# Performance work log

Measured on AMD Instinct MI355X. Metric: run time of the kernel, lower is better.

Reference implementation:

```python
import jax, jax.numpy as jnp
import numpy as np

L = 3          # num_gc_layers
DIM = 128      # hidden dim (== num_features)
BN_EPS = 1e-5


def _bn(h, gamma, beta):
    # torch BatchNorm1d training-mode normalization (biased variance)
    m = h.mean(axis=0)
    v = h.var(axis=0)
    return gamma * (h - m) * jax.lax.rsqrt(v + BN_EPS) + beta


def setup_inputs() -> dict:
    key = jax.random.key(0)
    ks = jax.random.split(key, 24)
    N, E, G = 50000, 600000, 256
    s = 0.05
    inp = {
        "x": jax.random.normal(ks[0], (N, DIM), jnp.float32),
        "src": jax.random.randint(ks[1], (E,), 0, N, jnp.int32),
        "dst": jax.random.randint(ks[2], (E,), 0, N, jnp.int32),
        "batch": jnp.sort(jax.random.randint(ks[3], (N,), 0, G, jnp.int32)),
        "n_graphs": G,
        # GIN MLP params (stacked over layers; num_features == dim)
        "conv_w1": jax.random.normal(ks[4], (L, DIM, DIM), jnp.float32) * s,
        "conv_b1": jnp.zeros((L, DIM), jnp.float32),
        "conv_w2": jax.random.normal(ks[5], (L, DIM, DIM), jnp.float32) * s,
        "conv_b2": jnp.zeros((L, DIM), jnp.float32),
        "bn_gamma": jnp.ones((L, DIM), jnp.float32),
        "bn_beta": jnp.zeros((L, DIM), jnp.float32),
        # summary weighter (dim -> 1)
        "sw_w": jax.random.normal(ks[6], (DIM, 1), jnp.float32) * s,
        "sw_b": jnp.zeros((1,), jnp.float32),
        # VAE heads
        "nmu_w": jax.random.normal(ks[7], (DIM, DIM), jnp.float32) * s,
        "nmu_b": jnp.zeros((DIM,), jnp.float32),
        "nlv_w": jax.random.normal(ks[8], (DIM, DIM), jnp.float32) * s,
        "nlv_b": jnp.zeros((DIM,), jnp.float32),
        "gmu_w": jax.random.normal(ks[9], (DIM, DIM), jnp.float32) * s,
        "gmu_b": jnp.zeros((DIM,), jnp.float32),
        "glv_w": jax.random.normal(ks[10], (DIM, DIM), jnp.float32) * s,
        "glv_b": jnp.zeros((DIM,), jnp.float32),
        # head BN params, order: [node_mu, node_logvar, graph_mu, graph_logvar]
        "head_gamma": jnp.ones((4, DIM), jnp.float32),
        "head_beta": jnp.zeros((4, DIM), jnp.float32),
    }
    return inp


def reference(x, src, dst, batch, n_graphs,
              conv_w1, conv_b1, conv_w2, conv_b2, bn_gamma, bn_beta,
              sw_w, sw_b, nmu_w, nmu_b, nlv_w, nlv_b,
              gmu_w, gmu_b, glv_w, glv_b, head_gamma, head_beta):
    N = x.shape[0]
    for i in range(L):
        # GINConv (eps=0): h = nn(x + sum_{j->i} x_j)
        agg = jax.ops.segment_sum(x[src], dst, num_segments=N)  # [N, dim]
        h = x + agg
        h = jax.nn.relu(h @ conv_w1[i] + conv_b1[i]) @ conv_w2[i] + conv_b2[i]
        x = _bn(jax.nn.relu(h), bn_gamma[i], bn_beta[i])

    w = jax.nn.sigmoid(x @ sw_w + sw_b)           # [N, 1]
    summary_info = w * x                          # [N, dim]
    noisy_info = (1.0 - w) * x                    # [N, dim]
    slots = jax.ops.segment_sum(summary_info, batch, num_segments=n_graphs)  # [G, dim]

    node_mu = _bn(jax.nn.relu(noisy_info @ nmu_w + nmu_b), head_gamma[0], head_beta[0])
    node_logvar = _bn(jax.nn.relu(noisy_info @ nlv_w + nlv_b), head_gamma[1], head_beta[1])
    graph_mu = _bn(jax.nn.relu(slots @ gmu_w + gmu_b), head_gamma[2], head_beta[2])
    graph_logvar = _bn(jax.nn.relu(slots @ glv_w + glv_b), head_gamma[3], head_beta[3])
    return (node_mu, node_logvar, graph_mu, graph_logvar)
```

## Files before the change

### kernel.cpp

```cpp
#include <hip/hip_runtime.h>
#include <hip/hip_bf16.h>

#define DIM 128
#define BN_EPS 1e-5f
#define NSTRIPE 32

typedef unsigned short ushortT;
typedef __attribute__((ext_vector_type(8))) short short8;
typedef __attribute__((ext_vector_type(4))) float floatx4;

__device__ __forceinline__ float bflo(unsigned u) { return __uint_as_float(u << 16); }
__device__ __forceinline__ float bfhi(unsigned u) { return __uint_as_float(u & 0xffff0000u); }
__device__ __forceinline__ float bf2f(ushortT h) { return __uint_as_float(((unsigned)h) << 16); }
__device__ __forceinline__ ushortT f2bf(float f) {
    unsigned x = __float_as_uint(f);
    unsigned r = (x + 0x7fff + ((x >> 16) & 1)) >> 16;
    return (ushortT)r;
}
__device__ __forceinline__ void decode8(const unsigned* ap, short8& hi, short8& lo) {
#pragma unroll
    for (int j = 0; j < 8; ++j) {
        hi[j] = (short)(ap[j] >> 16);
        lo[j] = (short)(ap[j] & 0xffffu);
    }
// ... 183 lines not shown
                const ushortT* sp = Xb + (size_t)eidx[i] * DIM + c0;
                acc8(&acc[0], *(const uint4*)(sp));
                acc8(&acc[8], *(const uint4*)(sp + 8));
            }
            if (sprev) {
                float cnt = (float)(e - b + 1);
#pragma unroll
                for (int jq = 0; jq < 4; ++jq) {
                    int c = c0 + jq * 4;
                    float4 sm = *(const float4*)&pstat[c];
                    float4 sq = *(const float4*)&pstat[128 + c];
                    float4 gm = *(const float4*)(gamma + c);
                    float4 bt = *(const float4*)(beta + c);
                    float m, sc;
                    m = sm.x * invM; sc = gm.x * rsqrtf(sq.x * invM - m * m + BN_EPS);
                    acc[jq * 4 + 0] = sc * acc[jq * 4 + 0] + cnt * (bt.x - sc * m);
                    m = sm.y * invM; sc = gm.y * rsqrtf(sq.y * invM - m * m + BN_EPS);
                    acc[jq * 4 + 1] = sc * acc[jq * 4 + 1] + cnt * (bt.y - sc * m);
                    m = sm.z * invM; sc = gm.z * rsqrtf(sq.z * invM - m * m + BN_EPS);
                    acc[jq * 4 + 2] = sc * acc[jq * 4 + 2] + cnt * (bt.z - sc * m);
                    m = sm.w * invM; sc = gm.w * rsqrtf(sq.w * invM - m * m + BN_EPS);
                    acc[jq * 4 + 3] = sc * acc[jq * 4 + 3] + cnt * (bt.w - sc * m);
                }
            }
        }
        unsigned pk[16];
#pragma unroll
        for (int j = 0; j < 16; ++j) {
            ushortT h = f2bf(acc[j]);
            ushortT l = f2bf(acc[j] - bf2f(h));
            pk[j] = ((unsigned)h << 16) | l;
        }
#pragma unroll
        for (int j4 = 0; j4 < 4; ++j4)
            *(uint4*)&As[nloc][c0 + j4 * 4] = *(uint4*)&pk[j4 * 4];
    }
    __syncthreads();

    int cbase = wave * 32;
    floatx4 acc[2][2];
#pragma unroll
    for (int mt = 0; mt < 2; ++mt)
#pragma unroll
        for (int nt = 0; nt < 2; ++nt)
            acc[mt][nt] = (floatx4){0.f, 0.f, 0.f, 0.f};

#pragma unroll
    for (int ks = 0; ks < 4; ++ks) {
        int k0 = ks * 32 + quad * 8;
        short8 bhi[2], blo[2];
#pragma unroll
        for (int nt = 0; nt < 2; ++nt) {
            const size_t woff = (size_t)(cbase + nt * 16 + l16) * DIM + k0;
            bhi[nt] = *(const short8*)(W1hi + woff);
            blo[nt] = *(const short8*)(W1lo + woff);
        }
#pragma unroll
        for (int mt = 0; mt < 2; ++mt) {
            int lr = mt * 16 + l16;
            unsigned ap[8];
            *(uint4*)&ap[0] = *(const uint4*)&As[lr][k0];
            *(uint4*)&ap[4] = *(const uint4*)&As[lr][k0 + 4];
            short8 ahi, alo;
            decode8(ap, ahi, alo);
#pragma unroll
            for (int nt = 0; nt < 2; ++nt) {
                acc[mt][nt] = __builtin_amdgcn_mfma_f32_16x16x32_bf16(ahi, bhi[nt], acc[mt][nt], 0, 0, 0);
                acc[mt][nt] = __builtin_amdgcn_mfma_f32_16x16x32_bf16(alo, bhi[nt], acc[mt][nt], 0, 0, 0);
                acc[mt][nt] = __builtin_amdgcn_mfma_f32_16x16x32_bf16(ahi, blo[nt], acc[mt][nt], 0, 0, 0);
            }
        }
    }
    __syncthreads();

#pragma unroll
    for (int nt = 0; nt < 2; ++nt) {
        int col = cbase + nt * 16 + l16;
        float bcol = b1[col];
#pragma unroll
        for (int mt = 0; mt < 2; ++mt)
#pragma unroll
            for (int r = 0; r < 4; ++r) {
                int lr = mt * 16 + quad * 4 + r;
                float v = fmaxf(acc[mt][nt][r] + bcol, 0.f);
                ushortT hv = f2bf(v);
                ushortT lv = f2bf(v - bf2f(hv));
                As[lr][col] = ((unsigned)hv << 16) | lv;
            }
    }
    __syncthreads();

#pragma unroll
    for (int mt = 0; mt < 2; ++mt)
#pragma unroll
        for (int nt = 0; nt < 2; ++nt)
            acc[mt][nt] = (floatx4){0.f, 0.f, 0.f, 0.f};

#pragma unroll
    for (int ks = 0; ks < 4; ++ks) {
        int k0 = ks * 32 + quad * 8;
        short8 bhi[2], blo[2];
#pragma unroll
        for (int nt = 0; nt < 2; ++nt) {
            const size_t woff = (size_t)(cbase + nt * 16 + l16) * DIM + k0;
            bhi[nt] = *(const short8*)(W2hi + woff);
            blo[nt] = *(const short8*)(W2lo + woff);
        }
#pragma unroll
        for (int mt = 0; mt < 2; ++mt) {
            int lr = mt * 16 + l16;
            unsigned ap[8];
            *(uint4*)&ap[0] = *(const uint4*)&As[lr][k0];
            *(uint4*)&ap[4] = *(const uint4*)&As[lr][k0 + 4];
            short8 ahi, alo;
            decode8(ap, ahi, alo);
#pragma unroll
            for (int nt = 0; nt < 2; ++nt) {
                acc[mt][nt] = __builtin_amdgcn_mfma_f32_16x16x32_bf16(ahi, bhi[nt], acc[mt][nt], 0, 0, 0);
                acc[mt][nt] = __builtin_amdgcn_mfma_f32_16x16x32_bf16(alo, bhi[nt], acc[mt][nt], 0, 0, 0);
                acc[mt][nt] = __builtin_amdgcn_mfma_f32_16x16x32_bf16(ahi, blo[nt], acc[mt][nt], 0, 0, 0);
            }
        }
    }
#pragma unroll
    for (int nt = 0; nt < 2; ++nt) {
        int col = cbase + nt * 16 + l16;
        float bcol = b2[col];
        float s = 0.f, sq = 0.f;
#pragma unroll
        for (int mt = 0; mt < 2; ++mt)
#pragma unroll
            for (int r = 0; r < 4; ++r) {
                int gr = m0 + mt * 16 + quad * 4 + r;
                if (gr < M) {
                    float v = fmaxf(acc[mt][nt][r] + bcol, 0.f);
                    rout[(size_t)gr * DIM + col] = f2bf(v);
                    s += v;
                    sq += v * v;
                }
            }
        s  += __shfl_xor(s, 16);  s  += __shfl_xor(s, 32);
        sq += __shfl_xor(sq, 16); sq += __shfl_xor(sq, 32);
        if (quad == 0) {
            atomicAdd(&ls[col], s);
            atomicAdd(&lsq[col], sq);
        }
    }
    __syncthreads();
    float* dstp = sdst + (size_t)(blockIdx.x & (NSTRIPE - 1)) * 256;
    if (t < 128) atomicAdd(&dstp[t], ls[t]);
    else         atomicAdd(&dstp[t], lsq[t - 128]);
}

__global__ __launch_bounds__(256) void heads_kernel(
    const unsigned* __restrict__ AP,
    const ushortT* __restrict__ WAhi, const ushortT* __restrict__ WAlo,
    const float* __restrict__ bA, ushortT* __restrict__ hA, float* __restrict__ sdstA,
    const ushortT* __restrict__ WBhi, const ushortT* __restrict__ WBlo,
    const float* __restrict__ bB, ushortT* __restrict__ hB, float* __restrict__ sdstB,
    int M)
{
    __shared__ float lsA[DIM], lsqA[DIM], lsB[DIM], lsqB[DIM];
    int t = threadIdx.x;
    int wave = t >> 6, lane = t & 63, quad = lane >> 4, l16 = lane & 15;
    int m0 = blockIdx.x * 64;
    int cbase = wave * 32;

    if (t < DIM) { lsA[t] = 0.f; lsqA[t] = 0.f; lsB[t] = 0.f; lsqB[t] = 0.f; }
    __syncthreads();

    floatx4 accA[4][2], accB[4][2];
#pragma unroll
    for (int mt = 0; mt < 4; ++mt)
#pragma unroll
        for (int nt = 0; nt < 2; ++nt) {
            accA[mt][nt] = (floatx4){0.f, 0.f, 0.f, 0.f};
            accB[mt][nt] = (floatx4){0.f, 0.f, 0.f, 0.f};
        }

    for (int ks = 0; ks < 4; ++ks) {
        int k0 = ks * 32 + quad * 8;
        short8 bAhi[2], bAlo[2], bBhi[2], bBlo[2];
#pragma unroll
        for (int nt = 0; nt < 2; ++nt) {
            const size_t woff = (size_t)(cbase + nt * 16 + l16) * DIM + k0;
            bAhi[nt] = *(const short8*)(WAhi + woff);
            bAlo[nt] = *(const short8*)(WAlo + woff);
            bBhi[nt] = *(const short8*)(WBhi + woff);
            bBlo[nt] = *(const short8*)(WBlo + woff);
        }
#pragma unroll
        for (int mt = 0; mt < 4; ++mt) {
            int row = m0 + mt * 16 + l16;
            unsigned ap[8] = {0, 0, 0, 0, 0, 0, 0, 0};
            if (row < M) {
                *(uint4*)&ap[0] = *(const uint4*)(AP + (size_t)row * DIM + k0);
                *(uint4*)&ap[4] = *(const uint4*)(AP + (size_t)row * DIM + k0 + 4);
            }
            short8 ahi, alo;
            decode8(ap, ahi, alo);
#pragma unroll
            for (int nt = 0; nt < 2; ++nt) {
                accA[mt][nt] = __builtin_amdgcn_mfma_f32_16x16x32_bf16(ahi, bAhi[nt], accA[mt][nt], 0, 0, 0);
                accA[mt][nt] = __builtin_amdgcn_mfma_f32_16x16x32_bf16(alo, bAhi[nt], accA[mt][nt], 0, 0, 0);
                accA[mt][nt] = __builtin_amdgcn_mfma_f32_16x16x32_bf16(ahi, bAlo[nt], accA[mt][nt], 0, 0, 0);
                accB[mt][nt] = __builtin_amdgcn_mfma_f32_16x16x32_bf16(ahi, bBhi[nt], accB[mt][nt], 0, 0, 0);
                accB[mt][nt] = __builtin_amdgcn_mfma_f32_16x16x32_bf16(alo, bBhi[nt], accB[mt][nt], 0, 0, 0);
                accB[mt][nt] = __builtin_amdgcn_mfma_f32_16x16x32_bf16(ahi, bBlo[nt], accB[mt][nt], 0, 0, 0);
            }
        }
    }

#pragma unroll
    for (int nt = 0; nt < 2; ++nt) {
        int col = cbase + nt * 16 + l16;
        float bcA = bA[col], bcB = bB[col];
        float sA = 0.f, sqA = 0.f, sB = 0.f, sqB = 0.f;
#pragma unroll
        for (int mt = 0; mt < 4; ++mt)
#pragma unroll
            for (int r = 0; r < 4; ++r) {
                int gr = m0 + mt * 16 + quad * 4 + r;
                if (gr < M) {
                    size_t off = (size_t)gr * DIM + col;
                    float vA = fmaxf(accA[mt][nt][r] + bcA, 0.f);
                    float vB = fmaxf(accB[mt][nt][r] + bcB, 0.f);
                    hA[off] = f2bf(vA);
                    hB[off] = f2bf(vB);
                    sA += vA; sqA += vA * vA;
                    sB += vB; sqB += vB * vB;
                }
            }
        sA += __shfl_xor(sA, 16);  sA += __shfl_xor(sA, 32);
        sqA += __shfl_xor(sqA, 16); sqA += __shfl_xor(sqA, 32);
        sB += __shfl_xor(sB, 16);  sB += __shfl_xor(sB, 32);
        sqB += __shfl_xor(sqB, 16); sqB += __shfl_xor(sqB, 32);
        if (quad == 0) {
            atomicAdd(&lsA[col], sA);
            atomicAdd(&lsqA[col], sqA);
            atomicAdd(&lsB[col], sB);
            atomicAdd(&lsqB[col], sqB);
        }
    }
    __syncthreads();
    int stripe = blockIdx.x & (NSTRIPE - 1);
    float* dA = sdstA + (size_t)stripe * 256;
    float* dB = sdstB + (size_t)stripe * 256;
    if (t < 128) { atomicAdd(&dA[t], lsA[t]); atomicAdd(&dB[t], lsB[t]); }
    else         { atomicAdd(&dA[t], lsqA[t - 128]); atomicAdd(&dB[t], lsqB[t - 128]); }
}

__global__ __launch_bounds__(256) void merge_stats2_kernel(
    const float* __restrict__ sA, float* __restrict__ oA,
    const float* __restrict__ sB, float* __restrict__ oB)
{
    const float* s = blockIdx.x ? sB : sA;
    float* o = blockIdx.x ? oB : oA;
    int t = threadIdx.x;
    float v = 0.f;
#pragma unroll
    for (int i = 0; i < NSTRIPE; ++i) v += s[i * 256 + t];
    o[t] = v;
}

__global__ __launch_bounds__(256) void gemm_graph_dual_kernel(
    const float* __restrict__ A32,
    const ushortT* __restrict__ W8hi, const ushortT* __restrict__ W8lo,
    const float* __restrict__ b8, float* __restrict__ C8, float* __restrict__ st8,
    const ushortT* __restrict__ W9hi, const ushortT* __restrict__ W9lo,
    const float* __restrict__ b9, float* __restrict__ C9, float* __restrict__ st9,
    int M, int nb)
{
    __shared__ float ls[DIM], lsq[DIM];
    int bb = blockIdx.x;
    const ushortT* Whi; const ushortT* Wlo; const float* bias; float* C; float* st;
    if (bb < nb) { Whi = W8hi; Wlo = W8lo; bias = b8; C = C8; st = st8; }
    else { bb -= nb; Whi = W9hi; Wlo = W9lo; bias = b9; C = C9; st = st9; }

    int t     = threadIdx.x;
    int wave  = t >> 6;
    int lane  = t & 63;
    int quad  = lane >> 4;
    int l16   = lane & 15;
    int m0    = bb * 64;
    int cbase = wave * 32;

    if (t < DIM) { ls[t] = 0.f; lsq[t] = 0.f; }
    __syncthreads();

    floatx4 acc[4][2];
#pragma unroll
    for (int mt = 0; mt < 4; ++mt)
#pragma unroll
        for (int nt = 0; nt < 2; ++nt)
            acc[mt][nt] = (floatx4){0.f, 0.f, 0.f, 0.f};

    for (int ks = 0; ks < 4; ++ks) {
        int k0 = ks * 32 + quad * 8;
        short8 bhi[2], blo[2];
#pragma unroll
        for (int nt = 0; nt < 2; ++nt) {
            const size_t woff = (size_t)(cbase + nt * 16 + l16) * DIM + k0;
            bhi[nt] = *(const short8*)(Whi + woff);
            blo[nt] = *(const short8*)(Wlo + woff);
        }
#pragma unroll
        for (int mt = 0; mt < 4; ++mt) {
            int row = m0 + mt * 16 + l16;
            short8 ahi = {0,0,0,0,0,0,0,0};
            short8 alo = {0,0,0,0,0,0,0,0};
            if (row < M) {
                float av[8];
                *(float4*)&av[0] = *(const float4*)(A32 + (size_t)row * DIM + k0);
                *(float4*)&av[4] = *(const float4*)(A32 + (size_t)row * DIM + k0 + 4);
#pragma unroll
                for (int j = 0; j < 8; ++j) {
                    ushortT hv = f2bf(av[j]);
                    ahi[j] = (short)hv;
                    alo[j] = (short)f2bf(av[j] - bf2f(hv));
                }
            }
#pragma unroll
            for (int nt = 0; nt < 2; ++nt) {
                acc[mt][nt] = __builtin_amdgcn_mfma_f32_16x16x32_bf16(ahi, bhi[nt], acc[mt][nt], 0, 0, 0);
                acc[mt][nt] = __builtin_amdgcn_mfma_f32_16x16x32_bf16(alo, bhi[nt], acc[mt][nt], 0, 0, 0);
                acc[mt][nt] = __builtin_amdgcn_mfma_f32_16x16x32_bf16(ahi, blo[nt], acc[mt][nt], 0, 0, 0);
            }
        }
    }

#pragma unroll
    for (int nt = 0; nt < 2; ++nt) {
        int col = cbase + nt * 16 + l16;
        float bcol = bias[col];
        float s = 0.f, sq = 0.f;
#pragma unroll
        for (int mt = 0; mt < 4; ++mt)
#pragma unroll
            for (int r = 0; r < 4; ++r) {
                int gr = m0 + mt * 16 + quad * 4 + r;
                if (gr < M) {
                    float v = fmaxf(acc[mt][nt][r] + bcol, 0.f);
                    C[(size_t)gr * DIM + col] = v;
                    s += v;
                    sq += v * v;
                }
            }
        s  += __shfl_xor(s, 16);  s  += __shfl_xor(s, 32);
        sq += __shfl_xor(sq, 16); sq += __shfl_xor(sq, 32);
        if (quad == 0) {
            atomicAdd(&ls[col], s);
            atomicAdd(&lsq[col], sq);
        }
    }
    __syncthreads();
    if (t < DIM) {
        atomicAdd(&st[t], ls[t]);
        atomicAdd(&st[DIM + t], lsq[t]);
    }
}

__global__ __launch_bounds__(256) void bn_dual_bf16_kernel(
    const ushortT* __restrict__ RA, float* __restrict__ OA, const float* __restrict__ stA,
    const float* __restrict__ gA, const float* __restrict__ bA,
    const ushortT* __restrict__ RB, float* __restrict__ OB, const float* __restrict__ stB,
    const float* __restrict__ gB, const float* __restrict__ bB,
    int M, int nb)
{
    int bb = blockIdx.x;
    const ushortT* R; float* O; const float* st; const float* gamma; const float* beta;
    if (bb < nb) { R = RA; O = OA; st = stA; gamma = gA; beta = bA; }
    else { bb -= nb; R = RB; O = OB; st = stB; gamma = gB; beta = bB; }
    int idx = bb * 256 + threadIdx.x;
    if (idx >= M * 32) return;
    int c4 = idx & 31;
    float invM = 1.0f / (float)M;
    uint2 u = ((const uint2*)R)[idx];
    float o[4] = {bflo(u.x), bfhi(u.x), bflo(u.y), bfhi(u.y)};
#pragma unroll
    for (int j = 0; j < 4; ++j) {
        int c = c4 * 4 + j;
        float m   = st[c] * invM;
        float var = st[DIM + c] * invM - m * m;
        float sc  = gamma[c] * rsqrtf(var + BN_EPS);
        o[j] = sc * (o[j] - m) + beta[c];
    }
    ((float4*)O)[idx] = make_float4(o[0], o[1], o[2], o[3]);
}

__global__ __launch_bounds__(256) void bn_dual_f32_kernel(
    float* __restrict__ CA, const float* __restrict__ stA,
    const float* __restrict__ gA, const float* __restrict__ bA,
    float* __restrict__ CB, const float* __restrict__ stB,
    const float* __restrict__ gB, const float* __restrict__ bB,
    int M, int nb)
{
    int bb = blockIdx.x;
    float* C; const float* st; const float* gamma; const float* beta;
    if (bb < nb) { C = CA; st = stA; gamma = gA; beta = bA; }
    else { bb -= nb; C = CB; st = stB; gamma = gB; beta = bB; }
    int idx = bb * 256 + threadIdx.x;
    if (idx >= M * 32) return;
    int c4 = idx & 31;
    float invM = 1.0f / (float)M;
    float4 v = ((const float4*)C)[idx];
    float o[4] = {v.x, v.y, v.z, v.w};
#pragma unroll
    for (int j = 0; j < 4; ++j) {
        int c = c4 * 4 + j;
        float m   = st[c] * invM;
        float var = st[DIM + c] * invM - m * m;
        float sc  = gamma[c] * rsqrtf(var + BN_EPS);
        o[j] = sc * (o[j] - m) + beta[c];
    }
    ((float4*)C)[idx] = make_float4(o[0], o[1], o[2], o[3]);
}

__global__ __launch_bounds__(256) void weigh_split_kernel(
    const ushortT* __restrict__ R, const int* __restrict__ batch,
    const float* __restrict__ sprev,
    const float* __restrict__ gamma, const float* __restrict__ beta,
    const float* __restrict__ sw_w, const float* __restrict__ sw_b,
    unsigned* __restrict__ noisyP, float* __restrict__ slots, int N, float invM)
{
    __shared__ float part[256];
    __shared__ float wsh[128];
    __shared__ float pstat[256];
    int t  = threadIdx.x;
    int r0 = blockIdx.x * 128;

    {
        float s = 0.f;
#pragma unroll
        for (int i = 0; i < NSTRIPE; ++i) s += sprev[i * 256 + t];
        pstat[t] = s;
    }
    __syncthreads();

    {
        int row  = r0 + (t >> 1);
        int cs   = (t & 1) * 64;
        float d = 0.f;
        if (row < N) {
            for (int c = cs; c < cs + 64; c += 4) {
                uint2 u = *(const uint2*)(R + (size_t)row * DIM + c);
                float rv[4] = {bflo(u.x), bfhi(u.x), bflo(u.y), bfhi(u.y)};
                float4 sm = *(const float4*)&pstat[c];
                float4 sq = *(const float4*)&pstat[128 + c];
                float4 gm = *(const float4*)(gamma + c);
                float4 bt = *(const float4*)(beta + c);
                float4 sw = *(const float4*)(sw_w + c);
                float m, sc;
                m = sm.x * invM; sc = gm.x * rsqrtf(sq.x * invM - m * m + BN_EPS);
                d += (sc * (rv[0] - m) + bt.x) * sw.x;
                m = sm.y * invM; sc = gm.y * rsqrtf(sq.y * invM - m * m + BN_EPS);
                d += (sc * (rv[1] - m) + bt.y) * sw.y;
                m = sm.z * invM; sc = gm.z * rsqrtf(sq.z * invM - m * m + BN_EPS);
                d += (sc * (rv[2] - m) + bt.z) * sw.z;
                m = sm.w * invM; sc = gm.w * rsqrtf(sq.w * invM - m * m + BN_EPS);
                d += (sc * (rv[3] - m) + bt.w) * sw.w;
            }
        }
        part[t] = d;
    }
    __syncthreads();
    if (t < 128) {
        float dd = part[2 * t] + part[2 * t + 1];
        wsh[t] = 1.0f / (1.0f + expf(-(dd + sw_b[0])));
    }
    __syncthreads();

    int c    = t & 127;
    int half = t >> 7;
    int rend = r0 + 128;
    if (rend > N) rend = N;
    float m   = pstat[c] * invM;
    float var = pstat[128 + c] * invM - m * m;
    float sc  = gamma[c] * rsqrtf(var + BN_EPS);
    float sh  = beta[c] - sc * m;
    int curg = -1;
    float acc = 0.f;
    for (int r = r0 + half; r < rend; r += 2) {
        float xv = sc * bf2f(R[(size_t)r * DIM + c]) + sh;
        float w  = wsh[r - r0];
        float nv = (1.f - w) * xv;
        ushortT hv = f2bf(nv);
        ushortT lv = f2bf(nv - bf2f(hv));
        noisyP[(size_t)r * DIM + c] = ((unsigned)hv << 16) | lv;
        int g = batch[r];
        if (g != curg) {
            if (curg >= 0) atomicAdd(&slots[(size_t)curg * DIM + c], acc);
            curg = g;
            acc = 0.f;
        }
        acc += w * xv;
    }
    if (curg >= 0) atomicAdd(&slots[(size_t)curg * DIM + c], acc);
}

extern "C" void kernel_launch(void* const* d_in, const int* in_sizes, int n_in,
                              void* d_out, int out_size, void* d_ws, size_t ws_size,
                              hipStream_t stream)
{
    const float* x      = (const float*)d_in[0];
    const int*   src    = (const int*)d_in[1];
    const int*   dst    = (const int*)d_in[2];
    const int*   batch  = (const int*)d_in[3];
    const float* cw1    = (const float*)d_in[5];
    const float* cb1    = (const float*)d_in[6];
    const float* cw2    = (const float*)d_in[7];
    const float* cb2    = (const float*)d_in[8];
    const float* bng    = (const float*)d_in[9];
    const float* bnb    = (const float*)d_in[10];
    const float* sw_w   = (const float*)d_in[11];
    const float* sw_b   = (const float*)d_in[12];
    const float* nmu_b  = (const float*)d_in[14];
    const float* nlv_b  = (const float*)d_in[16];
    const float* gmu_b  = (const float*)d_in[18];
    const float* glv_b  = (const float*)d_in[20];
    const float* hgam   = (const float*)d_in[21];
    const float* hbet   = (const float*)d_in[22];
    const float* nmu_w  = (const float*)d_in[13];
    const float* nlv_w  = (const float*)d_in[15];
    const float* gmu_w  = (const float*)d_in[17];
    const float* glv_w  = (const float*)d_in[19];

    const int N = in_sizes[0] / DIM;
    const int E = in_sizes[1];
    const int G = (out_size / DIM - 2 * N) / 2;

    float* out0 = (float*)d_out;
    float* out1 = out0 + (size_t)N * DIM;
    float* out2 = out1 + (size_t)N * DIM;
    float* out3 = out2 + (size_t)G * DIM;

    char* wp = (char*)d_ws;
    auto alloc = [&](size_t bytes) {
        char* p = wp;
        wp += (bytes + 255) & ~(size_t)255;
        return p;
    };
    ushortT*  xbf   = (ushortT*)alloc((size_t)N * DIM * 2);
    ushortT*  rA    = (ushortT*)alloc((size_t)N * DIM * 2);
    ushortT*  rB    = (ushortT*)alloc((size_t)N * DIM * 2);
    unsigned* noisyP= (unsigned*)alloc((size_t)N * DIM * 4);
    ushortT*  whi   = (ushortT*)alloc((size_t)10 * 16384 * 2);
    ushortT*  wlo   = (ushortT*)alloc((size_t)10 * 16384 * 2);
    float* slots    = (float*)alloc((size_t)G * DIM * 4);
    float* stats    = (float*)alloc((size_t)7 * 256 * 4);
    float* sbuf     = (float*)alloc((size_t)5 * NSTRIPE * 256 * 4);
    int* row_ptr    = (int*)alloc((size_t)(N + 2) * 4);
    int* eidx       = (int*)alloc((size_t)E * 4);
    int* deg   = (int*)noisyP;
    int* iscan = deg + N;
    int* bsum  = iscan + N;
    int* cur   = bsum + 256;

    auto SS = [&](int i) { return stats + (size_t)i * 256; };
    auto SB = [&](int i) { return sbuf + (size_t)i * NSTRIPE * 256; };

    const int edge_blocks  = (E + 255) / 256;
    const int scan_blocks  = (N + 255) / 256;
    const int layer_blocks = (N + 31) / 32;
    const int heads_blocks = (N + 63) / 64;
    const int g16_blocks   = (N * 16 + 255) / 256;
    const int g32_blocks   = (N * 32 + 255) / 256;
    const float invN = 1.0f / (float)N;

    const int sbufQ  = (5 * NSTRIPE * 256) / 4;
    const int slotsQ = (G * DIM) / 4;
    const int degQ   = (N + 3) / 4;
    const int statsQ = (7 * 256) / 4;
    const int zeroQ  = sbufQ + slotsQ + degQ + statsQ;
    const int zero_blocks = (zeroQ + 255) / 256;

    prep_kernel<<<640 + g16_blocks + zero_blocks, 256, 0, stream>>>(
        cw1, cw2, nmu_w, nlv_w, gmu_w, glv_w, whi, wlo,
        x, xbf, N * 16, g16_blocks,
        (float4*)sbuf, sbufQ, (float4*)slots, slotsQ,
        (float4*)deg, degQ, (float4*)stats, statsQ);

    hist_kernel<<<edge_blocks, 256, 0, stream>>>(dst, deg, E);
    scan1_kernel<<<scan_blocks, 256, 0, stream>>>(deg, iscan, bsum, N);
    scan2_kernel<<<1, 256, 0, stream>>>(bsum, scan_blocks);
    scan3_kernel<<<scan_blocks, 256, 0, stream>>>(iscan, bsum, deg, row_ptr, cur, N);
    fill_kernel<<<edge_blocks, 256, 0, stream>>>(src, dst, cur, eidx, E);

    const ushortT* lin[3]  = {xbf, rA, rB};
    ushortT*       lout[3] = {rA, rB, rA};
    for (int l = 0; l < 3; ++l) {
        const float* sprev  = (l == 0) ? nullptr : SB(l - 1);
        const float* g_prev = (l == 0) ? nullptr : bng + (size_t)(l - 1) * DIM;
        const float* b_prev = (l == 0) ? nullptr : bnb + (size_t)(l - 1) * DIM;
        layer_fused_kernel<<<layer_blocks, 256, 0, stream>>>(
            lin[l], row_ptr, eidx,
            sprev, g_prev, b_prev,
            whi + (size_t)l * 16384, wlo + (size_t)l * 16384, cb1 + (size_t)l * DIM,
            whi + (size_t)(3 + l) * 16384, wlo + (size_t)(3 + l) * 16384, cb2 + (size_t)l * DIM,
            lout[l], SB(l), N, invN);
    }
    ushortT* rfin = rA;
    ushortT* hA   = rB;
    ushortT* hB   = xbf;

    weigh_split_kernel<<<(N + 127) / 128, 256, 0, stream>>>(
        rfin, batch, SB(2), bng + 2 * DIM, bnb + 2 * DIM,
        sw_w, sw_b, noisyP, slots, N, invN);

    heads_kernel<<<heads_blocks, 256, 0, stream>>>(
        noisyP,
        whi + (size_t)6 * 16384, wlo + (size_t)6 * 16384, nmu_b, hA, SB(3),
        whi + (size_t)7 * 16384, wlo + (size_t)7 * 16384, nlv_b, hB, SB(4), N);
    merge_stats2_kernel<<<2, 256, 0, stream>>>(SB(3), SS(3), SB(4), SS(4));
    bn_dual_bf16_kernel<<<2 * g32_blocks, 256, 0, stream>>>(
        hA, out0, SS(3), hgam + 0 * DIM, hbet + 0 * DIM,
        hB, out1, SS(4), hgam + 1 * DIM, hbet + 1 * DIM, N, g32_blocks);

    const int gemm_blocks_G = (G + 63) / 64;
    const int gbn_blocks    = (G * 32 + 255) / 256;
    gemm_graph_dual_kernel<<<2 * gemm_blocks_G, 256, 0, stream>>>(
        slots,
        whi + (size_t)8 * 16384, wlo + (size_t)8 * 16384, gmu_b, out2, SS(5),
        whi + (size_t)9 * 16384, wlo + (size_t)9 * 16384, glv_b, out3, SS(6),
        G, gemm_blocks_G);
    bn_dual_f32_kernel<<<2 * gbn_blocks, 256, 0, stream>>>(
        out2, SS(5), hgam + 2 * DIM, hbet + 2 * DIM,
        out3, SS(6), hgam + 3 * DIM, hbet + 3 * DIM, G, gbn_blocks);
}
```

Baseline: 470.1 us.

## Fuse summary weighting into node head GEMM via shared-memory noisy tile

Merges the weigh/split kernel into the node-head GEMM kernel: each 64-row block computes the BN-normalized final features, the sigmoid weights and the slot sums, then writes the hi/lo-packed noisy features into an LDS tile that feeds the MFMA GEMM directly. This removes the global noisyP round trip (a 50000x128 uint32 write plus read) and one kernel launch. In exchange it uses a larger LDS footprint (about 34KB per block), which may reduce occupancy. It also halves the rows per block in the weighting phase, which doubles the per-block stripe-stat reduction and slot atomics.

```diff
diff --git a/kernel.cpp b/kernel.cpp
--- a/kernel.cpp
+++ b/kernel.cpp
@@ -359,282 +359,26 @@
     else         atomicAdd(&dstp[t], lsq[t - 128]);
 }
 
-__global__ __launch_bounds__(256) void heads_kernel(
-    const unsigned* __restrict__ AP,
+__global__ __launch_bounds__(256) void weigh_heads_kernel(
+    const ushortT* __restrict__ R, const int* __restrict__ batch,
+    const float* __restrict__ sprev,
+    const float* __restrict__ gamma, const float* __restrict__ beta,
+    const float* __restrict__ sw_w, const float* __restrict__ sw_b,
+    float* __restrict__ slots,
     const ushortT* __restrict__ WAhi, const ushortT* __restrict__ WAlo,
     const float* __restrict__ bA, ushortT* __restrict__ hA, float* __restrict__ sdstA,
     const ushortT* __restrict__ WBhi, const ushortT* __restrict__ WBlo,
     const float* __restrict__ bB, ushortT* __restrict__ hB, float* __restrict__ sdstB,
-    int M)
-{
+    int N, float invM)
+{
+    __shared__ unsigned As[64][DIM + 4];
+    __shared__ float pstat[256];
+    __shared__ float part[256];
+    __shared__ float wsh[64];
     __shared__ float lsA[DIM], lsqA[DIM], lsB[DIM], lsqB[DIM];
     int t = threadIdx.x;
     int wave = t >> 6, lane = t & 63, quad = lane >> 4, l16 = lane & 15;
     int m0 = blockIdx.x * 64;
-    int cbase = wave * 32;
-
-    if (t < DIM) { lsA[t] = 0.f; lsqA[t] = 0.f; lsB[t] = 0.f; lsqB[t] = 0.f; }
-    __syncthreads();
-
-    floatx4 accA[4][2], accB[4][2];
-#pragma unroll
-    for (int mt = 0; mt < 4; ++mt)
-#pragma unroll
-        for (int nt = 0; nt < 2; ++nt) {
-            accA[mt][nt] = (floatx4){0.f, 0.f, 0.f, 0.f};
-            accB[mt][nt] = (floatx4){0.f, 0.f, 0.f, 0.f};
-        }
-
-    for (int ks = 0; ks < 4; ++ks) {
-        int k0 = ks * 32 + quad * 8;
-        short8 bAhi[2], bAlo[2], bBhi[2], bBlo[2];
-#pragma unroll
-        for (int nt = 0; nt < 2; ++nt) {
-            const size_t woff = (size_t)(cbase + nt * 16 + l16) * DIM + k0;
-            bAhi[nt] = *(const short8*)(WAhi + woff);
-            bAlo[nt] = *(const short8*)(WAlo + woff);
-            bBhi[nt] = *(const short8*)(WBhi + woff);
-            bBlo[nt] = *(const short8*)(WBlo + woff);
-        }
-#pragma unroll
-        for (int mt = 0; mt < 4; ++mt) {
-            int row = m0 + mt * 16 + l16;
-            unsigned ap[8] = {0, 0, 0, 0, 0, 0, 0, 0};
-            if (row < M) {
-                *(uint4*)&ap[0] = *(const uint4*)(AP + (size_t)row * DIM + k0);
-                *(uint4*)&ap[4] = *(const uint4*)(AP + (size_t)row * DIM + k0 + 4);
-            }
-            short8 ahi, alo;
-            decode8(ap, ahi, alo);
-#pragma unroll
-            for (int nt = 0; nt < 2; ++nt) {
-                accA[mt][nt] = __builtin_amdgcn_mfma_f32_16x16x32_bf16(ahi, bAhi[nt], accA[mt][nt], 0, 0, 0);
-                accA[mt][nt] = __builtin_amdgcn_mfma_f32_16x16x32_bf16(alo, bAhi[nt], accA[mt][nt], 0, 0, 0);
-                accA[mt][nt] = __builtin_amdgcn_mfma_f32_16x16x32_bf16(ahi, bAlo[nt], accA[mt][nt], 0, 0, 0);
-                accB[mt][nt] = __builtin_amdgcn_mfma_f32_16x16x32_bf16(ahi, bBhi[nt], accB[mt][nt], 0, 0, 0);
-                accB[mt][nt] = __builtin_amdgcn_mfma_f32_16x16x32_bf16(alo, bBhi[nt], accB[mt][nt], 0, 0, 0);
-                accB[mt][nt] = __builtin_amdgcn_mfma_f32_16x16x32_bf16(ahi, bBlo[nt], accB[mt][nt], 0, 0, 0);
-            }
-        }
-    }
-
-#pragma unroll
-    for (int nt = 0; nt < 2; ++nt) {
-        int col = cbase + nt * 16 + l16;
-        float bcA = bA[col], bcB = bB[col];
-        float sA = 0.f, sqA = 0.f, sB = 0.f, sqB = 0.f;
-#pragma unroll
-        for (int mt = 0; mt < 4; ++mt)
-#pragma unroll
-            for (int r = 0; r < 4; ++r) {
-                int gr = m0 + mt * 16 + quad * 4 + r;
-                if (gr < M) {
-                    size_t off = (size_t)gr * DIM + col;
-                    float vA = fmaxf(accA[mt][nt][r] + bcA, 0.f);
-                    float vB = fmaxf(accB[mt][nt][r] + bcB, 0.f);
-                    hA[off] = f2bf(vA);
-                    hB[off] = f2bf(vB);
-                    sA += vA; sqA += vA * vA;
-                    sB += vB; sqB += vB * vB;
-                }
-            }
-        sA += __shfl_xor(sA, 16);  sA += __shfl_xor(sA, 32);
-        sqA += __shfl_xor(sqA, 16); sqA += __shfl_xor(sqA, 32);
-        sB += __shfl_xor(sB, 16);  sB += __shfl_xor(sB, 32);
-        sqB += __shfl_xor(sqB, 16); sqB += __shfl_xor(sqB, 32);
-        if (quad == 0) {
-            atomicAdd(&lsA[col], sA);
-            atomicAdd(&lsqA[col], sqA);
-            atomicAdd(&lsB[col], sB);
-            atomicAdd(&lsqB[col], sqB);
-        }
-    }
-    __syncthreads();
-    int stripe = blockIdx.x & (NSTRIPE - 1);
-    float* dA = sdstA + (size_t)stripe * 256;
-    float* dB = sdstB + (size_t)stripe * 256;
-    if (t < 128) { atomicAdd(&dA[t], lsA[t]); atomicAdd(&dB[t], lsB[t]); }
-    else         { atomicAdd(&dA[t], lsqA[t - 128]); atomicAdd(&dB[t], lsqB[t - 128]); }
-}
-
-__global__ __launch_bounds__(256) void merge_stats2_kernel(
-    const float* __restrict__ sA, float* __restrict__ oA,
-    const float* __restrict__ sB, float* __restrict__ oB)
-{
-    const float* s = blockIdx.x ? sB : sA;
-    float* o = blockIdx.x ? oB : oA;
-    int t = threadIdx.x;
-    float v = 0.f;
-#pragma unroll
-    for (int i = 0; i < NSTRIPE; ++i) v += s[i * 256 + t];
-    o[t] = v;
-}
-
-__global__ __launch_bounds__(256) void gemm_graph_dual_kernel(
-    const float* __restrict__ A32,
-    const ushortT* __restrict__ W8hi, const ushortT* __restrict__ W8lo,
-    const float* __restrict__ b8, float* __restrict__ C8, float* __restrict__ st8,
-    const ushortT* __restrict__ W9hi, const ushortT* __restrict__ W9lo,
-    const float* __restrict__ b9, float* __restrict__ C9, float* __restrict__ st9,
-    int M, int nb)
-{
-    __shared__ float ls[DIM], lsq[DIM];
-    int bb = blockIdx.x;
-    const ushortT* Whi; const ushortT* Wlo; const float* bias; float* C; float* st;
-    if (bb < nb) { Whi = W8hi; Wlo = W8lo; bias = b8; C = C8; st = st8; }
-    else { bb -= nb; Whi = W9hi; Wlo = W9lo; bias = b9; C = C9; st = st9; }
-
-    int t     = threadIdx.x;
-    int wave  = t >> 6;
-    int lane  = t & 63;
-    int quad  = lane >> 4;
-    int l16   = lane & 15;
-    int m0    = bb * 64;
-    int cbase = wave * 32;
-
-    if (t < DIM) { ls[t] = 0.f; lsq[t] = 0.f; }
-    __syncthreads();
-
-    floatx4 acc[4][2];
-#pragma unroll
-    for (int mt = 0; mt < 4; ++mt)
-#pragma unroll
-        for (int nt = 0; nt < 2; ++nt)
-            acc[mt][nt] = (floatx4){0.f, 0.f, 0.f, 0.f};
-
-    for (int ks = 0; ks < 4; ++ks) {
-        int k0 = ks * 32 + quad * 8;
-        short8 bhi[2], blo[2];
-#pragma unroll
-        for (int nt = 0; nt < 2; ++nt) {
-            const size_t woff = (size_t)(cbase + nt * 16 + l16) * DIM + k0;
-            bhi[nt] = *(const short8*)(Whi + woff);
-            blo[nt] = *(const short8*)(Wlo + woff);
-        }
-#pragma unroll
-        for (int mt = 0; mt < 4; ++mt) {
-            int row = m0 + mt * 16 + l16;
-            short8 ahi = {0,0,0,0,0,0,0,0};
-            short8 alo = {0,0,0,0,0,0,0,0};
-            if (row < M) {
-                float av[8];
-                *(float4*)&av[0] = *(const float4*)(A32 + (size_t)row * DIM + k0);
-                *(float4*)&av[4] = *(const float4*)(A32 + (size_t)row * DIM + k0 + 4);
-#pragma unroll
-                for (int j = 0; j < 8; ++j) {
-                    ushortT hv = f2bf(av[j]);
-                    ahi[j] = (short)hv;
-                    alo[j] = (short)f2bf(av[j] - bf2f(hv));
-                }
-            }
-#pragma unroll
-            for (int nt = 0; nt < 2; ++nt) {
-                acc[mt][nt] = __builtin_amdgcn_mfma_f32_16x16x32_bf16(ahi, bhi[nt], acc[mt][nt], 0, 0, 0);
-                acc[mt][nt] = __builtin_amdgcn_mfma_f32_16x16x32_bf16(alo, bhi[nt], acc[mt][nt], 0, 0, 0);
-                acc[mt][nt] = __builtin_amdgcn_mfma_f32_16x16x32_bf16(ahi, blo[nt], acc[mt][nt], 0, 0, 0);
-            }
-        }
-    }
-
-#pragma unroll
-    for (int nt = 0; nt < 2; ++nt) {
-        int col = cbase + nt * 16 + l16;
-        float bcol = bias[col];
-        float s = 0.f, sq = 0.f;
-#pragma unroll
-        for (int mt = 0; mt < 4; ++mt)
-#pragma unroll
-            for (int r = 0; r < 4; ++r) {
-                int gr = m0 + mt * 16 + quad * 4 + r;
-                if (gr < M) {
-                    float v = fmaxf(acc[mt][nt][r] + bcol, 0.f);
-                    C[(size_t)gr * DIM + col] = v;
-                    s += v;
-                    sq += v * v;
-                }
-            }
-        s  += __shfl_xor(s, 16);  s  += __shfl_xor(s, 32);
-        sq += __shfl_xor(sq, 16); sq += __shfl_xor(sq, 32);
-        if (quad == 0) {
-            atomicAdd(&ls[col], s);
-            atomicAdd(&lsq[col], sq);
-        }
-    }
-    __syncthreads();
-    if (t < DIM) {
-        atomicAdd(&st[t], ls[t]);
-        atomicAdd(&st[DIM + t], lsq[t]);
-    }
-}
-
-__global__ __launch_bounds__(256) void bn_dual_bf16_kernel(
-    const ushortT* __restrict__ RA, float* __restrict__ OA, const float* __restrict__ stA,
-    const float* __restrict__ gA, const float* __restrict__ bA,
-    const ushortT* __restrict__ RB, float* __restrict__ OB, const float* __restrict__ stB,
-    const float* __restrict__ gB, const float* __restrict__ bB,
-    int M, int nb)
-{
-    int bb = blockIdx.x;
-    const ushortT* R; float* O; const float* st; const float* gamma; const float* beta;
-    if (bb < nb) { R = RA; O = OA; st = stA; gamma = gA; beta = bA; }
-    else { bb -= nb; R = RB; O = OB; st = stB; gamma = gB; beta = bB; }
-    int idx = bb * 256 + threadIdx.x;
-    if (idx >= M * 32) return;
-    int c4 = idx & 31;
-    float invM = 1.0f / (float)M;
-    uint2 u = ((const uint2*)R)[idx];
-    float o[4] = {bflo(u.x), bfhi(u.x), bflo(u.y), bfhi(u.y)};
-#pragma unroll
-    for (int j = 0; j < 4; ++j) {
-        int c = c4 * 4 + j;
-        float m   = st[c] * invM;
-        float var = st[DIM + c] * invM - m * m;
-        float sc  = gamma[c] * rsqrtf(var + BN_EPS);
-        o[j] = sc * (o[j] - m) + beta[c];
-    }
-    ((float4*)O)[idx] = make_float4(o[0], o[1], o[2], o[3]);
-}
-
-__global__ __launch_bounds__(256) void bn_dual_f32_kernel(
-    float* __restrict__ CA, const float* __restrict__ stA,
-    const float* __restrict__ gA, const float* __restrict__ bA,
-    float* __restrict__ CB, const float* __restrict__ stB,
-    const float* __restrict__ gB, const float* __restrict__ bB,
-    int M, int nb)
-{
-    int bb = blockIdx.x;
-    float* C; const float* st; const float* gamma; const float* beta;
-    if (bb < nb) { C = CA; st = stA; gamma = gA; beta = bA; }
-    else { bb -= nb; C = CB; st = stB; gamma = gB; beta = bB; }
-    int idx = bb * 256 + threadIdx.x;
-    if (idx >= M * 32) return;
-    int c4 = idx & 31;
-    float invM = 1.0f / (float)M;
-    float4 v = ((const float4*)C)[idx];
-    float o[4] = {v.x, v.y, v.z, v.w};
-#pragma unroll
-    for (int j = 0; j < 4; ++j) {
-        int c = c4 * 4 + j;
-        float m   = st[c] * invM;
-        float var = st[DIM + c] * invM - m * m;
-        float sc  = gamma[c] * rsqrtf(var + BN_EPS);
-        o[j] = sc * (o[j] - m) + beta[c];
-    }
-    ((float4*)C)[idx] = make_float4(o[0], o[1], o[2], o[3]);
-}
-
-__global__ __launch_bounds__(256) void weigh_split_kernel(
-    const ushortT* __restrict__ R, const int* __restrict__ batch,
-    const float* __restrict__ sprev,
-    const float* __restrict__ gamma, const float* __restrict__ beta,
-    const float* __restrict__ sw_w, const float* __restrict__ sw_b,
-    unsigned* __restrict__ noisyP, float* __restrict__ slots, int N, float invM)
-{
-    __shared__ float part[256];
-    __shared__ float wsh[128];
-    __shared__ float pstat[256];
-    int t  = threadIdx.x;
-    int r0 = blockIdx.x * 128;
 
     {
         float s = 0.f;
@@ -642,14 +386,15 @@
         for (int i = 0; i < NSTRIPE; ++i) s += sprev[i * 256 + t];
         pstat[t] = s;
     }
+    if (t < DIM) { lsA[t] = 0.f; lsqA[t] = 0.f; lsB[t] = 0.f; lsqB[t] = 0.f; }
     __syncthreads();
 
     {
-        int row  = r0 + (t >> 1);
-        int cs   = (t & 1) * 64;
+        int row = m0 + (t >> 2);
+        int cs  = (t & 3) * 32;
         float d = 0.f;
         if (row < N) {
-            for (int c = cs; c < cs + 64; c += 4) {
+            for (int c = cs; c < cs + 32; c += 4) {
                 uint2 u = *(const uint2*)(R + (size_t)row * DIM + c);
                 float rv[4] = {bflo(u.x), bfhi(u.x), bflo(u.y), bfhi(u.y)};
                 float4 sm = *(const float4*)&pstat[c];
@@ -671,38 +416,289 @@
         part[t] = d;
     }
     __syncthreads();
-    if (t < 128) {
-        float dd = part[2 * t] + part[2 * t + 1];
+    if (t < 64) {
+        float dd = part[4 * t] + part[4 * t + 1] + part[4 * t + 2] + part[4 * t + 3];
         wsh[t] = 1.0f / (1.0f + expf(-(dd + sw_b[0])));
     }
     __syncthreads();
 
-    int c    = t & 127;
-    int half = t >> 7;
-    int rend = r0 + 128;
-    if (rend > N) rend = N;
-    float m   = pstat[c] * invM;
-    float var = pstat[128 + c] * invM - m * m;
-    float sc  = gamma[c] * rsqrtf(var + BN_EPS);
-    float sh  = beta[c] - sc * m;
-    int curg = -1;
-    float acc = 0.f;
-    for (int r = r0 + half; r < rend; r += 2) {
-        float xv = sc * bf2f(R[(size_t)r * DIM + c]) + sh;
-        float w  = wsh[r - r0];
-        float nv = (1.f - w) * xv;
-        ushortT hv = f2bf(nv);
-        ushortT lv = f2bf(nv - bf2f(hv));
-        noisyP[(size_t)r * DIM + c] = ((unsigned)hv << 16) | lv;
-        int g = batch[r];
-        if (g != curg) {
-            if (curg >= 0) atomicAdd(&slots[(size_t)curg * DIM + c], acc);
-            curg = g;
-            acc = 0.f;
-        }
-        acc += w * xv;
-    }
-    if (curg >= 0) atomicAdd(&slots[(size_t)curg * DIM + c], acc);
+    {
+        int c    = t & 127;
+        int half = t >> 7;
+        float m   = pstat[c] * invM;
+        float var = pstat[128 + c] * invM - m * m;
+        float sc  = gamma[c] * rsqrtf(var + BN_EPS);
+        float sh  = beta[c] - sc * m;
+        int curg = -1;
+        float acc = 0.f;
+        for (int r = half; r < 64; r += 2) {
+            int row = m0 + r;
+            if (row < N) {
+                float xv = sc * bf2f(R[(size_t)row * DIM + c]) + sh;
+                float w  = wsh[r];
+                float nv = (1.f - w) * xv;
+                ushortT hv = f2bf(nv);
+                ushortT lv = f2bf(nv - bf2f(hv));
+                As[r][c] = ((unsigned)hv << 16) | lv;
+                int g = batch[row];
+                if (g != curg) {
+                    if (curg >= 0) atomicAdd(&slots[(size_t)curg * DIM + c], acc);
+                    curg = g;
+                    acc = 0.f;
+                }
+                acc += w * xv;
+            } else {
+                As[r][c] = 0;
+            }
+        }
+        if (curg >= 0) atomicAdd(&slots[(size_t)curg * DIM + c], acc);
+    }
+    __syncthreads();
+
+    int cbase = wave * 32;
+    floatx4 accA[4][2], accB[4][2];
+#pragma unroll
+    for (int mt = 0; mt < 4; ++mt)
+#pragma unroll
+        for (int nt = 0; nt < 2; ++nt) {
+            accA[mt][nt] = (floatx4){0.f, 0.f, 0.f, 0.f};
+            accB[mt][nt] = (floatx4){0.f, 0.f, 0.f, 0.f};
+        }
+
+    for (int ks = 0; ks < 4; ++ks) {
+        int k0 = ks * 32 + quad * 8;
+        short8 bAhi[2], bAlo[2], bBhi[2], bBlo[2];
+#pragma unroll
+        for (int nt = 0; nt < 2; ++nt) {
+            const size_t woff = (size_t)(cbase + nt * 16 + l16) * DIM + k0;
+            bAhi[nt] = *(const short8*)(WAhi + woff);
+            bAlo[nt] = *(const short8*)(WAlo + woff);
+            bBhi[nt] = *(const short8*)(WBhi + woff);
+            bBlo[nt] = *(const short8*)(WBlo + woff);
+        }
+#pragma unroll
+        for (int mt = 0; mt < 4; ++mt) {
+            int lr = mt * 16 + l16;
+            unsigned ap[8];
+            *(uint4*)&ap[0] = *(const uint4*)&As[lr][k0];
+            *(uint4*)&ap[4] = *(const uint4*)&As[lr][k0 + 4];
+            short8 ahi, alo;
+            decode8(ap, ahi, alo);
+#pragma unroll
+            for (int nt = 0; nt < 2; ++nt) {
+                accA[mt][nt] = __builtin_amdgcn_mfma_f32_16x16x32_bf16(ahi, bAhi[nt], accA[mt][nt], 0, 0, 0);
+                accA[mt][nt] = __builtin_amdgcn_mfma_f32_16x16x32_bf16(alo, bAhi[nt], accA[mt][nt], 0, 0, 0);
+                accA[mt][nt] = __builtin_amdgcn_mfma_f32_16x16x32_bf16(ahi, bAlo[nt], accA[mt][nt], 0, 0, 0);
+                accB[mt][nt] = __builtin_amdgcn_mfma_f32_16x16x32_bf16(ahi, bBhi[nt], accB[mt][nt], 0, 0, 0);
+                accB[mt][nt] = __builtin_amdgcn_mfma_f32_16x16x32_bf16(alo, bBhi[nt], accB[mt][nt], 0, 0, 0);
+                accB[mt][nt] = __builtin_amdgcn_mfma_f32_16x16x32_bf16(ahi, bBlo[nt], accB[mt][nt], 0, 0, 0);
+            }
+        }
+    }
+
+#pragma unroll
+    for (int nt = 0; nt < 2; ++nt) {
+        int col = cbase + nt * 16 + l16;
+        float bcA = bA[col], bcB = bB[col];
+        float sA = 0.f, sqA = 0.f, sB = 0.f, sqB = 0.f;
+#pragma unroll
+        for (int mt = 0; mt < 4; ++mt)
+#pragma unroll
+            for (int r = 0; r < 4; ++r) {
+                int gr = m0 + mt * 16 + quad * 4 + r;
+                if (gr < N) {
+                    size_t off = (size_t)gr * DIM + col;
+                    float vA = fmaxf(accA[mt][nt][r] + bcA, 0.f);
+                    float vB = fmaxf(accB[mt][nt][r] + bcB, 0.f);
+                    hA[off] = f2bf(vA);
+                    hB[off] = f2bf(vB);
+                    sA += vA; sqA += vA * vA;
+                    sB += vB; sqB += vB * vB;
+                }
+            }
+        sA += __shfl_xor(sA, 16);  sA += __shfl_xor(sA, 32);
+        sqA += __shfl_xor(sqA, 16); sqA += __shfl_xor(sqA, 32);
+        sB += __shfl_xor(sB, 16);  sB += __shfl_xor(sB, 32);
+        sqB += __shfl_xor(sqB, 16); sqB += __shfl_xor(sqB, 32);
+        if (quad == 0) {
+            atomicAdd(&lsA[col], sA);
+            atomicAdd(&lsqA[col], sqA);
+            atomicAdd(&lsB[col], sB);
+            atomicAdd(&lsqB[col], sqB);
+        }
+    }
+    __syncthreads();
+    int stripe = blockIdx.x & (NSTRIPE - 1);
+    float* dA = sdstA + (size_t)stripe * 256;
+    float* dB = sdstB + (size_t)stripe * 256;
+    if (t < 128) { atomicAdd(&dA[t], lsA[t]); atomicAdd(&dB[t], lsB[t]); }
+    else         { atomicAdd(&dA[t], lsqA[t - 128]); atomicAdd(&dB[t], lsqB[t - 128]); }
+}
+
+__global__ __launch_bounds__(256) void merge_stats2_kernel(
+    const float* __restrict__ sA, float* __restrict__ oA,
+    const float* __restrict__ sB, float* __restrict__ oB)
+{
+    const float* s = blockIdx.x ? sB : sA;
+    float* o = blockIdx.x ? oB : oA;
+    int t = threadIdx.x;
+    float v = 0.f;
+#pragma unroll
+    for (int i = 0; i < NSTRIPE; ++i) v += s[i * 256 + t];
+    o[t] = v;
+}
+
+__global__ __launch_bounds__(256) void gemm_graph_dual_kernel(
+    const float* __restrict__ A32,
+    const ushortT* __restrict__ W8hi, const ushortT* __restrict__ W8lo,
+    const float* __restrict__ b8, float* __restrict__ C8, float* __restrict__ st8,
+    const ushortT* __restrict__ W9hi, const ushortT* __restrict__ W9lo,
+    const float* __restrict__ b9, float* __restrict__ C9, float* __restrict__ st9,
+    int M, int nb)
+{
+    __shared__ float ls[DIM], lsq[DIM];
+    int bb = blockIdx.x;
+    const ushortT* Whi; const ushortT* Wlo; const float* bias; float* C; float* st;
+    if (bb < nb) { Whi = W8hi; Wlo = W8lo; bias = b8; C = C8; st = st8; }
+    else { bb -= nb; Whi = W9hi; Wlo = W9lo; bias = b9; C = C9; st = st9; }
+
+    int t     = threadIdx.x;
+    int wave  = t >> 6;
+    int lane  = t & 63;
+    int quad  = lane >> 4;
+    int l16   = lane & 15;
+    int m0    = bb * 64;
+    int cbase = wave * 32;
+
+    if (t < DIM) { ls[t] = 0.f; lsq[t] = 0.f; }
+    __syncthreads();
+
+    floatx4 acc[4][2];
+#pragma unroll
+    for (int mt = 0; mt < 4; ++mt)
+#pragma unroll
+        for (int nt = 0; nt < 2; ++nt)
+            acc[mt][nt] = (floatx4){0.f, 0.f, 0.f, 0.f};
+
+    for (int ks = 0; ks < 4; ++ks) {
+        int k0 = ks * 32 + quad * 8;
+        short8 bhi[2], blo[2];
+#pragma unroll
+        for (int nt = 0; nt < 2; ++nt) {
+            const size_t woff = (size_t)(cbase + nt * 16 + l16) * DIM + k0;
+            bhi[nt] = *(const short8*)(Whi + woff);
+            blo[nt] = *(const short8*)(Wlo + woff);
+        }
+#pragma unroll
+        for (int mt = 0; mt < 4; ++mt) {
+            int row = m0 + mt * 16 + l16;
+            short8 ahi = {0,0,0,0,0,0,0,0};
+            short8 alo = {0,0,0,0,0,0,0,0};
+            if (row < M) {
+                float av[8];
+                *(float4*)&av[0] = *(const float4*)(A32 + (size_t)row * DIM + k0);
+                *(float4*)&av[4] = *(const float4*)(A32 + (size_t)row * DIM + k0 + 4);
+#pragma unroll
+                for (int j = 0; j < 8; ++j) {
+                    ushortT hv = f2bf(av[j]);
+                    ahi[j] = (short)hv;
+                    alo[j] = (short)f2bf(av[j] - bf2f(hv));
+                }
+            }
+#pragma unroll
+            for (int nt = 0; nt < 2; ++nt) {
+                acc[mt][nt] = __builtin_amdgcn_mfma_f32_16x16x32_bf16(ahi, bhi[nt], acc[mt][nt], 0, 0, 0);
+                acc[mt][nt] = __builtin_amdgcn_mfma_f32_16x16x32_bf16(alo, bhi[nt], acc[mt][nt], 0, 0, 0);
+                acc[mt][nt] = __builtin_amdgcn_mfma_f32_16x16x32_bf16(ahi, blo[nt], acc[mt][nt], 0, 0, 0);
+            }
+        }
+    }
+
+#pragma unroll
+    for (int nt = 0; nt < 2; ++nt) {
+        int col = cbase + nt * 16 + l16;
+        float bcol = bias[col];
+        float s = 0.f, sq = 0.f;
+#pragma unroll
+        for (int mt = 0; mt < 4; ++mt)
+#pragma unroll
+            for (int r = 0; r < 4; ++r) {
+                int gr = m0 + mt * 16 + quad * 4 + r;
+                if (gr < M) {
+                    float v = fmaxf(acc[mt][nt][r] + bcol, 0.f);
+                    C[(size_t)gr * DIM + col] = v;
+                    s += v;
+                    sq += v * v;
+                }
+            }
+        s  += __shfl_xor(s, 16);  s  += __shfl_xor(s, 32);
+        sq += __shfl_xor(sq, 16); sq += __shfl_xor(sq, 32);
+        if (quad == 0) {
+            atomicAdd(&ls[col], s);
+            atomicAdd(&lsq[col], sq);
+        }
+    }
+    __syncthreads();
+    if (t < DIM) {
+        atomicAdd(&st[t], ls[t]);
+        atomicAdd(&st[DIM + t], lsq[t]);
+    }
+}
+
+__global__ __launch_bounds__(256) void bn_dual_bf16_kernel(
+    const ushortT* __restrict__ RA, float* __restrict__ OA, const float* __restrict__ stA,
+    const float* __restrict__ gA, const float* __restrict__ bA,
+    const ushortT* __restrict__ RB, float* __restrict__ OB, const float* __restrict__ stB,
+    const float* __restrict__ gB, const float* __restrict__ bB,
+    int M, int nb)
+{
+    int bb = blockIdx.x;
+    const ushortT* R; float* O; const float* st; const float* gamma; const float* beta;
+    if (bb < nb) { R = RA; O = OA; st = stA; gamma = gA; beta = bA; }
+    else { bb -= nb; R = RB; O = OB; st = stB; gamma = gB; beta = bB; }
+    int idx = bb * 256 + threadIdx.x;
+    if (idx >= M * 32) return;
+    int c4 = idx & 31;
+    float invM = 1.0f / (float)M;
+    uint2 u = ((const uint2*)R)[idx];
+    float o[4] = {bflo(u.x), bfhi(u.x), bflo(u.y), bfhi(u.y)};
+#pragma unroll
+    for (int j = 0; j < 4; ++j) {
+        int c = c4 * 4 + j;
+        float m   = st[c] * invM;
+        float var = st[DIM + c] * invM - m * m;
+        float sc  = gamma[c] * rsqrtf(var + BN_EPS);
+        o[j] = sc * (o[j] - m) + beta[c];
+    }
+    ((float4*)O)[idx] = make_float4(o[0], o[1], o[2], o[3]);
+}
+
+__global__ __launch_bounds__(256) void bn_dual_f32_kernel(
+    float* __restrict__ CA, const float* __restrict__ stA,
+    const float* __restrict__ gA, const float* __restrict__ bA,
+    float* __restrict__ CB, const float* __restrict__ stB,
+    const float* __restrict__ gB, const float* __restrict__ bB,
+    int M, int nb)
+{
+    int bb = blockIdx.x;
+    float* C; const float* st; const float* gamma; const float* beta;
+    if (bb < nb) { C = CA; st = stA; gamma = gA; beta = bA; }
+    else { bb -= nb; C = CB; st = stB; gamma = gB; beta = bB; }
+    int idx = bb * 256 + threadIdx.x;
+    if (idx >= M * 32) return;
+    int c4 = idx & 31;
+    float invM = 1.0f / (float)M;
+    float4 v = ((const float4*)C)[idx];
+    float o[4] = {v.x, v.y, v.z, v.w};
+#pragma unroll
+    for (int j = 0; j < 4; ++j) {
+        int c = c4 * 4 + j;
+        float m   = st[c] * invM;
+        float var = st[DIM + c] * invM - m * m;
+        float sc  = gamma[c] * rsqrtf(var + BN_EPS);
+        o[j] = sc * (o[j] - m) + beta[c];
+    }
+    ((float4*)C)[idx] = make_float4(o[0], o[1], o[2], o[3]);
 }
 
 extern "C" void kernel_launch(void* const* d_in, const int* in_sizes, int n_in,
@@ -810,14 +806,12 @@
     ushortT* hA   = rB;
     ushortT* hB   = xbf;
 
-    weigh_split_kernel<<<(N + 127) / 128, 256, 0, stream>>>(
+    weigh_heads_kernel<<<heads_blocks, 256, 0, stream>>>(
         rfin, batch, SB(2), bng + 2 * DIM, bnb + 2 * DIM,
-        sw_w, sw_b, noisyP, slots, N, invN);
-
-    heads_kernel<<<heads_blocks, 256, 0, stream>>>(
-        noisyP,
+        sw_w, sw_b, slots,
         whi + (size_t)6 * 16384, wlo + (size_t)6 * 16384, nmu_b, hA, SB(3),
-        whi + (size_t)7 * 16384, wlo + (size_t)7 * 16384, nlv_b, hB, SB(4), N);
+        whi + (size_t)7 * 16384, wlo + (size_t)7 * 16384, nlv_b, hB, SB(4),
+        N, invN);
     merge_stats2_kernel<<<2, 256, 0, stream>>>(SB(3), SS(3), SB(4), SS(4));
     bn_dual_bf16_kernel<<<2 * g32_blocks, 256, 0, stream>>>(
         hA, out0, SS(3), hgam + 0 * DIM, hbet + 0 * DIM,
```

New measurement: 455.0 us. -3.2%, faster.
